# Performance work log

Measured on AMD Instinct MI355X. Metric: run time of the kernel, lower is better.

Reference implementation:

```python
import jax, jax.numpy as jnp
import numpy as np

NEG_SLOPE = 0.2
EPS = 1e-16


def gat_layer(x, src, dst, W, att_src, att_dst, bias, heads, out_ch, concat, n_nodes):
    # Linear projection -> [N, H, C]
    h = (x @ W).reshape(n_nodes, heads, out_ch)
    # Per-node attention logits [N, H]
    a_src = (h * att_src[None]).sum(-1)
    a_dst = (h * att_dst[None]).sum(-1)
    # Per-edge logits, LeakyReLU (message j -> i with src=j, dst=i)
    alpha = a_src[src] + a_dst[dst]                      # [E, H]
    alpha = jnp.where(alpha >= 0, alpha, NEG_SLOPE * alpha)
    # Segment softmax over incoming edges of each dst node
    amax = jax.ops.segment_max(alpha, dst, num_segments=n_nodes)  # [N, H]
    ealpha = jnp.exp(alpha - amax[dst])
    denom = jax.ops.segment_sum(ealpha, dst, num_segments=n_nodes)
    alpha = ealpha / (denom[dst] + EPS)
    # Weighted messages + scatter-add aggregation
    msg = h[src] * alpha[..., None]                      # [E, H, C]
    out = jax.ops.segment_sum(msg, dst, num_segments=n_nodes)  # [N, H, C]
    out = out.reshape(n_nodes, heads * out_ch) if concat else out.mean(axis=1)
    return out + bias


def setup_inputs() -> dict:
    key = jax.random.key(0)
    ks = jax.random.split(key, 11)
    N, E, F, H, C1 = 50000, 1600000, 128, 8, 8
    x = jax.random.normal(ks[0], (N, F), dtype=jnp.float32)
    edge_index = jax.random.randint(ks[1], (2, E), 0, N, dtype=jnp.int64)
    s = 1.0 / np.sqrt(F)
    W1 = jax.random.normal(ks[2], (F, H * C1), dtype=jnp.float32) * s
    att_src1 = jax.random.normal(ks[3], (H, C1), dtype=jnp.float32) * 0.1
    att_dst1 = jax.random.normal(ks[4], (H, C1), dtype=jnp.float32) * 0.1
    bias1 = jax.random.normal(ks[5], (H * C1,), dtype=jnp.float32) * 0.1
    W2 = jax.random.normal(ks[6], (H * C1, F), dtype=jnp.float32) * (1.0 / np.sqrt(H * C1))
    att_src2 = jax.random.normal(ks[7], (1, F), dtype=jnp.float32) * 0.1
    att_dst2 = jax.random.normal(ks[8], (1, F), dtype=jnp.float32) * 0.1
    bias2 = jax.random.normal(ks[9], (F,), dtype=jnp.float32) * 0.1
    return {"x": x, "edge_index": edge_index, "W1": W1, "att_src1": att_src1,
            "att_dst1": att_dst1, "bias1": bias1, "W2": W2, "att_src2": att_src2,
            "att_dst2": att_dst2, "bias2": bias2}


def reference(x, edge_index, W1, att_src1, att_dst1, bias1, W2, att_src2, att_dst2, bias2):
    N = x.shape[0]
    # PyG GATConv add_self_loops=True: append (i, i) for every node
    loops = jnp.arange(N, dtype=edge_index.dtype)
    src = jnp.concatenate([edge_index[0], loops])
    dst = jnp.concatenate([edge_index[1], loops])
    # eval mode: dropouts are identity
    h = gat_layer(x, src, dst, W1, att_src1, att_dst1, bias1, heads=8, out_ch=8,
                  concat=True, n_nodes=N)            # [N, 64]
    h = jax.nn.elu(h)
    out = gat_layer(h, src, dst, W2, att_src2, att_dst2, bias2, heads=1, out_ch=128,
                    concat=False, n_nodes=N)         # [N, 128]
    return out
```

## Files before the change

kernel.cpp:

```cpp
#include <hip/hip_runtime.h>
#include <stdint.h>

#define NEG_SLOPE 0.2f
#define EPSV 1e-16f
#define LOG2E 1.44269504088896340736f
#define NBLK 256
#define BCAP 12288
#define PKCAP 8192

typedef __attribute__((ext_vector_type(8))) _Float16 half8;
typedef __attribute__((ext_vector_type(4))) float f32x4;

__device__ inline void get_edge(const void* ei, int is64, int E, int e, int& s, int& d){
  if (e >= E){ s = d = e - E; return; }
  if (is64){
    const long long* p = (const long long*)ei;
    s = (int)p[e]; d = (int)p[(long long)E + e];
  } else {
    const int* p = (const int*)ei;
    s = p[e]; d = p[E + e];
  }
}

__global__ __launch_bounds__(256) void k1g(const void* ei,
                     const float* __restrict__ x,
                     const float* __restrict__ W1,
                     const float* __restrict__ att_s, const float* __restrict__ att_d,
                     _Float16* __restrict__ Cb,
                     float* __restrict__ asrc1, float* __restrict__ adst1, int M,
                     const float* __restrict__ W2, _Float16* __restrict__ W2p,
                     const float* __restrict__ as2, const float* __restrict__ ad2,
                     float* __restrict__ va_s, float* __restrict__ va_d,
                     int E, int E2, int GG,
                     int* __restrict__ gcnt,
                     unsigned* __restrict__ packed){
  __shared__ char smem[34*1024];
  int b = blockIdx.x, t = threadIdx.x;

  if (b < GG){
    _Float16* Bs = (_Float16*)smem;
#pragma unroll
    for (int r = 0; r < 32; ++r){
      int idx = r*256 + t;
      int j = idx & 7, n16 = (idx >> 3) & 15, q = (idx >> 7) & 3, tile = idx >> 9;
      int nt = tile & 3, kt = tile >> 2;
      int k = kt*32 + q*8 + j, n = nt*16 + n16;
      Bs[idx] = (_Float16)W1[k*64 + n];
    }
    __syncthreads();
    int wave = (b*256 + t) >> 6;
    int lane = t & 63;
    int row0 = wave << 4;
    if (row0 >= M) return;
    int m = lane & 15, q = lane >> 4;
    f32x4 acc[4];
#pragma unroll
    for (int i = 0; i < 4; ++i) acc[i] = (f32x4){0.f,0.f,0.f,0.f};
#pragma unroll
    for (int kt = 0; kt < 4; ++kt){
      const float* xr = x + (size_t)(row0 + m)*128 + kt*32 + q*8;
      f32x4 f0 = *(const f32x4*)xr;
      f32x4 f1 = *(const f32x4*)(xr + 4);
      half8 a;
#pragma unroll
      for (int j = 0; j < 4; ++j){ a[j] = (_Float16)f0[j]; a[4 + j] = (_Float16)f1[j]; }
#pragma unroll
      for (int nt = 0; nt < 4; ++nt){
        half8 bfr = *(const half8*)(Bs + (size_t)(((kt*4 + nt)*4 + q)*16 + m)*8);
        acc[nt] = __builtin_amdgcn_mfma_f32_16x16x32_f16(a, bfr, acc[nt], 0, 0, 0);
      }
    }
#pragma unroll
    for (int nt = 0; nt < 4; ++nt){
#pragma unroll
      for (int r = 0; r < 4; ++r){
        Cb[(size_t)(row0 + q*4 + r)*64 + nt*16 + m] = (_Float16)acc[nt][r];
      }
    }
    float atts[4], attd[4];
#pragma unroll
    for (int nt = 0; nt < 4; ++nt){
      atts[nt] = att_s[nt*16 + m] * LOG2E;
      attd[nt] = att_d[nt*16 + m] * LOG2E;
    }
    int isw = (m & 7) == 0;
#pragma unroll
    for (int r = 0; r < 4; ++r){
      int row = row0 + q*4 + r;
#pragma unroll
      for (int nt = 0; nt < 4; ++nt){
        float ps = acc[nt][r] * atts[nt];
        float pd = acc[nt][r] * attd[nt];
#pragma unroll
        for (int mm = 1; mm <= 4; mm <<= 1){
          ps += __shfl_xor(ps, mm, 64);
          pd += __shfl_xor(pd, mm, 64);
        }
        if (isw){
          int head = 2*nt + (m >> 3);
          asrc1[row*8 + head] = ps;
          adst1[row*8 + head] = pd;
        }
      }
    }
    return;
  }

  if (b == GG){
#pragma unroll
    for (int r = 0; r < 32; ++r){
      int idx = r*256 + t;
      int j = idx & 7, n16 = (idx >> 3) & 15, q = (idx >> 7) & 3, tile = idx >> 9;
      int nt = tile & 7, kt = tile >> 3;
      int k = kt*32 + q*8 + j, n = nt*16 + n16;
      W2p[idx] = (_Float16)W2[k*128 + n];
    }
    if (t < 64){
      float s = 0.f, d = 0.f;
      for (int c = 0; c < 128; ++c){
        float w = W2[t*128 + c];
        s = fmaf(w, as2[c], s);
        d = fmaf(w, ad2[c], d);
      }
      va_s[t] = s * LOG2E; va_d[t] = d * LOG2E;
    }
    return;
  }

  unsigned* pk = (unsigned*)smem;
  int* h   = (int*)(smem + 32*1024);
  int* cur = (int*)(smem + 33*1024);
  int blk = b - GG - 1;
  int chunk = (E2 + NBLK - 1)/NBLK;
  int beg = blk*chunk, end = min(beg + chunk, E2), cnt = end - beg;
  const int* e32 = (const int*)ei;
  int nz = 0;
  for (int i = 0; i < 64; ++i) nz |= e32[2*i + 1];
  int is64 = (nz == 0) ? 1 : 0;
  h[t] = 0; __syncthreads();
  for (int j = t; j < cnt; j += 256){
    int s, d; get_edge(ei, is64, E, beg + j, s, d);
    unsigned p = ((unsigned)s << 16) | (unsigned)d;
    pk[j] = p;
    atomicAdd(&h[(p >> 8) & 255u], 1);
  }
  __syncthreads();
  int mine = h[t];
  int base_t = 0;
  if (mine > 0) base_t = atomicAdd(&gcnt[t*16], mine);
  cur[t] = base_t;
  __syncthreads();
  for (int j = t; j < cnt; j += 256){
    unsigned p = pk[j];
    int bk = (p >> 8) & 255u;
    int pos = atomicAdd(&cur[bk], 1);
    packed[(size_t)bk*BCAP + pos] = p;
  }
}

__global__ __launch_bounds__(256) void gemm2(const _Float16* __restrict__ A, const _Float16* __restrict__ Bp,
                                             const float* __restrict__ bias,
                                             float* __restrict__ C, int M){
  constexpr int NKT = 2, NNT = 8;
  int wave = (blockIdx.x*256 + (int)threadIdx.x) >> 6;
  int lane = threadIdx.x & 63;
  int row0 = wave << 4;
  if (row0 >= M) return;
  int m = lane & 15, q = lane >> 4;
  f32x4 acc[NNT];
#pragma unroll
  for (int i = 0; i < NNT; ++i) acc[i] = (f32x4){0.f,0.f,0.f,0.f};
#pragma unroll
  for (int kt = 0; kt < NKT; ++kt){
    half8 a = *(const half8*)(A + (size_t)(row0 + m)*64 + kt*32 + q*8);
#pragma unroll
    for (int nt = 0; nt < NNT; ++nt){
      half8 b = *(const half8*)(Bp + (size_t)(((kt*NNT + nt)*4 + q)*16 + m)*8);
      acc[nt] = __builtin_amdgcn_mfma_f32_16x16x32_f16(a, b, acc[nt], 0, 0, 0);
    }
  }
#pragma unroll
  for (int nt = 0; nt < NNT; ++nt){
    float bv = bias[nt*16 + m];
#pragma unroll
    for (int r = 0; r < 4; ++r){
      C[(size_t)(row0 + q*4 + r)*128 + nt*16 + m] = acc[nt][r] + bv;
    }
  }
}

__global__ __launch_bounds__(256) void p4_sort(const unsigned* __restrict__ packed,
                                               const int* __restrict__ gcnt,
                                               int N, int E2,
                                               int* __restrict__ offs, int* __restrict__ srcs){
  __shared__ int hist[256];
  __shared__ int cur[256];
  __shared__ int tot[256];
  __shared__ int sbase, scnt;
  int b = blockIdx.x, t = threadIdx.x;
  int v0 = gcnt[t*16];
  tot[t] = v0; __syncthreads();
  for (int off = 1; off < 256; off <<= 1){
    int v = (t >= off) ? tot[t - off] : 0;
    __syncthreads(); tot[t] += v; __syncthreads();
  }
  if (t == b){ sbase = tot[t] - v0; scnt = v0; }
  __syncthreads();
  int base = sbase, cnt = scnt;
  hist[t] = 0; __syncthreads();
  const unsigned* bp = packed + (size_t)b*BCAP;
  for (int p = t; p < cnt; p += 256){
    atomicAdd(&hist[bp[p] & 255u], 1);
  }
  __syncthreads();
  int v = hist[t];
  cur[t] = v; __syncthreads();
  for (int off = 1; off < 256; off <<= 1){
    int u = (t >= off) ? cur[t - off] : 0;
    __syncthreads(); cur[t] += u; __syncthreads();
  }
  int ex = cur[t] - v;
  __syncthreads();
  cur[t] = ex;
  int node = b*256 + t;
  if (node < N) offs[node] = base + ex;
  __syncthreads();
  for (int p = t; p < cnt; p += 256){
    unsigned pk = bp[p];
    int pos = atomicAdd(&cur[pk & 255u], 1);
    srcs[base + pos] = (int)((pk >> 16) << 7);
  }
  if (b == 0 && t == 0) offs[N] = E2;
}

__global__ __launch_bounds__(256) void agg_l1(const char* __restrict__ h1b,
                       const float* __restrict__ asrc, const float* __restrict__ adst,
                       const int* __restrict__ offs, const int* __restrict__ srcs,
                       const float* __restrict__ bias,
                       const float* __restrict__ va_s, const float* __restrict__ va_d,
                       uint4* __restrict__ hout,
                       float* __restrict__ asrc2, float* __restrict__ adst2, int N){
  int tid = threadIdx.x;
  int i = blockIdx.x*4 + (tid >> 6);
  if (i >= N) return;
  int lane = tid & 63, g = lane >> 3, c = lane & 7;
  unsigned coff = (unsigned)(c << 4);
  float ad = adst[i*8 + c];
  int beg = offs[i], end = offs[i + 1], last = end - 1;
  float acc[8];
#pragma unroll
  for (int k = 0; k < 8; ++k) acc[k] = 0.f;
  float den = 0.f;
  float a[4]; half8 v[4];
  {
    unsigned so[4];
#pragma unroll
    for (int k = 0; k < 4; ++k) so[k] = (unsigned)srcs[min(beg + 8*k + g, last)];
#pragma unroll
    for (int k = 0; k < 4; ++k) a[k] = asrc[(so[k] >> 4) + (unsigned)c];
#pragma unroll
    for (int k = 0; k < 4; ++k) v[k] = *(const half8*)(h1b + (size_t)(so[k] + coff));
  }
  for (int p = beg; p < end; p += 32){
    int pn = p + 32;
    unsigned so_n[4]; float a_n[4]; half8 v_n[4];
#pragma unroll
    for (int k = 0; k < 4; ++k) so_n[k] = (unsigned)srcs[min(pn + 8*k + g, last)];
#pragma unroll
    for (int k = 0; k < 4; ++k) a_n[k] = asrc[(so_n[k] >> 4) + (unsigned)c];
#pragma unroll
    for (int k = 0; k < 4; ++k) v_n[k] = *(const half8*)(h1b + (size_t)(so_n[k] + coff));
    float w[4];
#pragma unroll
    for (int k = 0; k < 4; ++k){
      float z = a[k] + ad;
      z = fmaxf(z, NEG_SLOPE*z);
      w[k] = (p + 8*k + g < end) ? exp2f(z) : 0.f;
      den += w[k];
    }
#pragma unroll
    for (int k = 0; k < 4; ++k){
#pragma unroll
      for (int j = 0; j < 8; ++j){
        acc[j] = fmaf((float)v[k][j], w[k], acc[j]);
      }
    }
#pragma unroll
    for (int k = 0; k < 4; ++k){ a[k] = a_n[k]; v[k] = v_n[k]; }
  }
#pragma unroll
  for (int mm = 8; mm <= 32; mm <<= 1){
#pragma unroll
    for (int k = 0; k < 8; ++k) acc[k] += __shfl_xor(acc[k], mm, 64);
    den += __shfl_xor(den, mm, 64);
  }
  if (g == 0){
    float inv = 1.f/(den + EPSV);
    float o[8];
    union { _Float16 h[8]; uint4 u; } ov;
#pragma unroll
    for (int k = 0; k < 8; ++k){
      float t = acc[k]*inv + bias[c*8 + k];
      t = (t > 0.f) ? t : (__expf(t) - 1.f);
      o[k] = t;
      ov.h[k] = (_Float16)t;
    }
    hout[(size_t)i*8 + c] = ov.u;
    float ps = 0.f, pd = 0.f;
#pragma unroll
    for (int k = 0; k < 8; ++k){
      ps = fmaf(o[k], va_s[c*8 + k], ps);
      pd = fmaf(o[k], va_d[c*8 + k], pd);
    }
#pragma unroll
    for (int mm = 1; mm <= 4; mm <<= 1){
      ps += __shfl_xor(ps, mm, 8);
      pd += __shfl_xor(pd, mm, 8);
    }
    if (c == 0){ asrc2[i] = ps; adst2[i] = pd; }
  }
}

__global__ __launch_bounds__(256) void agg_l2(const char* __restrict__ hin2,
                       const float* __restrict__ asrc, const float* __restrict__ adst,
                       const int* __restrict__ offs, const int* __restrict__ srcs,
                       uint4* __restrict__ qout, int N){
  int tid = threadIdx.x;
  int i = blockIdx.x*4 + (tid >> 6);
  if (i >= N) return;
  int lane = tid & 63, g = lane >> 3, c = lane & 7;
  unsigned coff = (unsigned)(c << 4);
  float ad = adst[i];
  int beg = offs[i], end = offs[i + 1], last = end - 1;
  float acc[8];
#pragma unroll
  for (int k = 0; k < 8; ++k) acc[k] = 0.f;
  float den = 0.f;
  float a[4]; half8 v[4];
  {
    unsigned so[4];
#pragma unroll
    for (int k = 0; k < 4; ++k) so[k] = (unsigned)srcs[min(beg + 8*k + g, last)];
#pragma unroll
    for (int k = 0; k < 4; ++k) a[k] = asrc[so[k] >> 7];
#pragma unroll
    for (int k = 0; k < 4; ++k) v[k] = *(const half8*)(hin2 + (size_t)(so[k] + coff));
  }
  for (int p = beg; p < end; p += 32){
    int pn = p + 32;
    unsigned so_n[4]; float a_n[4]; half8 v_n[4];
#pragma unroll
    for (int k = 0; k < 4; ++k) so_n[k] = (unsigned)srcs[min(pn + 8*k + g, last)];
#pragma unroll
    for (int k = 0; k < 4; ++k) a_n[k] = asrc[so_n[k] >> 7];
#pragma unroll
    for (int k = 0; k < 4; ++k) v_n[k] = *(const half8*)(hin2 + (size_t)(so_n[k] + coff));
    float w[4];
#pragma unroll
    for (int k = 0; k < 4; ++k){
      float z = a[k] + ad;
      z = fmaxf(z, NEG_SLOPE*z);
      w[k] = (p + 8*k + g < end) ? exp2f(z) : 0.f;
      den += w[k];
    }
#pragma unroll
    for (int k = 0; k < 4; ++k){
#pragma unroll
      for (int j = 0; j < 8; ++j){
        acc[j] = fmaf((float)v[k][j], w[k], acc[j]);
      }
    }
#pragma unroll
    for (int k = 0; k < 4; ++k){ a[k] = a_n[k]; v[k] = v_n[k]; }
  }
#pragma unroll
  for (int mm = 8; mm <= 32; mm <<= 1){
#pragma unroll
    for (int k = 0; k < 8; ++k) acc[k] += __shfl_xor(acc[k], mm, 64);
    den += __shfl_xor(den, mm, 64);
  }
  if (g == 0){
    float inv = 1.f/(den + EPSV);
    union { _Float16 h[8]; uint4 u; } ov;
#pragma unroll
    for (int k = 0; k < 8; ++k) ov.h[k] = (_Float16)(acc[k]*inv);
    qout[(size_t)i*8 + c] = ov.u;
  }
}

extern "C" void kernel_launch(void* const* d_in, const int* in_sizes, int n_in,
                              void* d_out, int out_size, void* d_ws, size_t ws_size,
                              hipStream_t stream){
  const float* x   = (const float*)d_in[0];
  const void*  ei  = d_in[1];
  const float* W1  = (const float*)d_in[2];
  const float* as1 = (const float*)d_in[3];
  const float* ad1 = (const float*)d_in[4];
  const float* b1  = (const float*)d_in[5];
  const float* W2  = (const float*)d_in[6];
  const float* as2 = (const float*)d_in[7];
  const float* ad2 = (const float*)d_in[8];
  const float* b2  = (const float*)d_in[9];

  int N  = in_sizes[0] / 128;
  int E  = in_sizes[1] / 2;
  int E2 = E + N;
  int NB = (N + 255) >> 8;

  char* p = (char*)d_ws;
  auto alloc = [&](size_t bytes) -> void* {
    void* r = (void*)p;
    p += (bytes + 255) & ~(size_t)255;
    return r;
  };
  _Float16* W2p    = (_Float16*)alloc((size_t)64*128*2);
  _Float16* h1b    = (_Float16*)alloc((size_t)N*64*2);
  float*    asrc1  = (float*)alloc((size_t)N*8*4);
  float*    adst1  = (float*)alloc((size_t)N*8*4);
  _Float16* hin2   = (_Float16*)alloc((size_t)N*64*2);
  _Float16* hq     = (_Float16*)alloc((size_t)N*64*2);
  float*    asrc2  = (float*)alloc((size_t)N*4);
  float*    adst2  = (float*)alloc((size_t)N*4);
  float*    va_s2  = (float*)alloc(64*4);
  float*    va_d2  = (float*)alloc(64*4);
  int*      offs   = (int*)alloc((size_t)(N + 1)*4);
  int*      srcs   = (int*)alloc((size_t)E2*4);
  unsigned* packed = (unsigned*)alloc((size_t)256*BCAP*4);
  int*      gcnt   = (int*)alloc((size_t)256*16*4);

  dim3 B(256);
  hipMemsetAsync(gcnt, 0, (size_t)256*16*4, stream);

  int nwav = (N + 15)/16;
  int GG = (nwav + 3)/4;

  k1g<<<GG + 1 + NBLK, B, 0, stream>>>(ei, x, W1, as1, ad1, h1b, asrc1, adst1, N,
                                       W2, W2p, as2, ad2, va_s2, va_d2,
                                       E, E2, GG, gcnt, packed);

  p4_sort<<<NB, B, 0, stream>>>(packed, gcnt, N, E2, offs, srcs);

  agg_l1<<<(N + 3)/4, B, 0, stream>>>((const char*)h1b, asrc1, adst1, offs, srcs, b1,
                                      va_s2, va_d2, (uint4*)hin2, asrc2, adst2, N);

  agg_l2<<<(N + 3)/4, B, 0, stream>>>((const char*)hin2, asrc2, adst2, offs, srcs,
                                      (uint4*)hq, N);

  gemm2<<<(nwav + 3)/4, B, 0, stream>>>(hq, W2p, b2, (float*)d_out, N);
}
```

Baseline: 240.7 us.

## Fuse layer-2 aggregation with output projection and drop software prefetch

Merges the layer-2 aggregation kernel with the final 64x128 projection. Each block aggregates four nodes into shared memory, then computes the 128 outputs per node with scalar FMAs against a transposed fp16 W2, plus bias. This removes the intermediate fp16 buffer round trip and one kernel launch, but gives up the MFMA GEMM for scalar math. It also drops the register double-buffered prefetch of edge data in both aggregation loops, which lowers register pressure but may expose gather latency.

```diff
diff --git a/kernel.cpp b/kernel.cpp
--- a/kernel.cpp
+++ b/kernel.cpp
@@ -28,7 +28,7 @@
                      const float* __restrict__ att_s, const float* __restrict__ att_d,
                      _Float16* __restrict__ Cb,
                      float* __restrict__ asrc1, float* __restrict__ adst1, int M,
-                     const float* __restrict__ W2, _Float16* __restrict__ W2p,
+                     const float* __restrict__ W2, _Float16* __restrict__ W2t,
                      const float* __restrict__ as2, const float* __restrict__ ad2,
                      float* __restrict__ va_s, float* __restrict__ va_d,
                      int E, int E2, int GG,
@@ -110,10 +110,8 @@
 #pragma unroll
     for (int r = 0; r < 32; ++r){
       int idx = r*256 + t;
-      int j = idx & 7, n16 = (idx >> 3) & 15, q = (idx >> 7) & 3, tile = idx >> 9;
-      int nt = tile & 7, kt = tile >> 3;
-      int k = kt*32 + q*8 + j, n = nt*16 + n16;
-      W2p[idx] = (_Float16)W2[k*128 + n];
+      int j = idx >> 6, c = idx & 63;
+      W2t[idx] = (_Float16)W2[c*128 + j];
     }
     if (t < 64){
       float s = 0.f, d = 0.f;
@@ -158,37 +156,6 @@
   }
 }
 
-__global__ __launch_bounds__(256) void gemm2(const _Float16* __restrict__ A, const _Float16* __restrict__ Bp,
-                                             const float* __restrict__ bias,
-                                             float* __restrict__ C, int M){
-  constexpr int NKT = 2, NNT = 8;
-  int wave = (blockIdx.x*256 + (int)threadIdx.x) >> 6;
-  int lane = threadIdx.x & 63;
-  int row0 = wave << 4;
-  if (row0 >= M) return;
-  int m = lane & 15, q = lane >> 4;
-  f32x4 acc[NNT];
-#pragma unroll
-  for (int i = 0; i < NNT; ++i) acc[i] = (f32x4){0.f,0.f,0.f,0.f};
-#pragma unroll
-  for (int kt = 0; kt < NKT; ++kt){
-    half8 a = *(const half8*)(A + (size_t)(row0 + m)*64 + kt*32 + q*8);
-#pragma unroll
-    for (int nt = 0; nt < NNT; ++nt){
-      half8 b = *(const half8*)(Bp + (size_t)(((kt*NNT + nt)*4 + q)*16 + m)*8);
-      acc[nt] = __builtin_amdgcn_mfma_f32_16x16x32_f16(a, b, acc[nt], 0, 0, 0);
-    }
-  }
-#pragma unroll
-  for (int nt = 0; nt < NNT; ++nt){
-    float bv = bias[nt*16 + m];
-#pragma unroll
-    for (int r = 0; r < 4; ++r){
-      C[(size_t)(row0 + q*4 + r)*128 + nt*16 + m] = acc[nt][r] + bv;
-    }
-  }
-}
-
 __global__ __launch_bounds__(256) void p4_sort(const unsigned* __restrict__ packed,
                                                const int* __restrict__ gcnt,
                                                int N, int E2,
@@ -251,31 +218,24 @@
 #pragma unroll
   for (int k = 0; k < 8; ++k) acc[k] = 0.f;
   float den = 0.f;
-  float a[4]; half8 v[4];
-  {
-    unsigned so[4];
-#pragma unroll
-    for (int k = 0; k < 4; ++k) so[k] = (unsigned)srcs[min(beg + 8*k + g, last)];
+  for (int p = beg; p < end; p += 32){
+    int m[4]; unsigned so[4];
+#pragma unroll
+    for (int k = 0; k < 4; ++k) m[k] = p + 8*k + g;
+#pragma unroll
+    for (int k = 0; k < 4; ++k) so[k] = (unsigned)srcs[min(m[k], last)];
+    float a[4];
 #pragma unroll
     for (int k = 0; k < 4; ++k) a[k] = asrc[(so[k] >> 4) + (unsigned)c];
+    half8 v[4];
 #pragma unroll
     for (int k = 0; k < 4; ++k) v[k] = *(const half8*)(h1b + (size_t)(so[k] + coff));
-  }
-  for (int p = beg; p < end; p += 32){
-    int pn = p + 32;
-    unsigned so_n[4]; float a_n[4]; half8 v_n[4];
-#pragma unroll
-    for (int k = 0; k < 4; ++k) so_n[k] = (unsigned)srcs[min(pn + 8*k + g, last)];
-#pragma unroll
-    for (int k = 0; k < 4; ++k) a_n[k] = asrc[(so_n[k] >> 4) + (unsigned)c];
-#pragma unroll
-    for (int k = 0; k < 4; ++k) v_n[k] = *(const half8*)(h1b + (size_t)(so_n[k] + coff));
     float w[4];
 #pragma unroll
     for (int k = 0; k < 4; ++k){
       float z = a[k] + ad;
       z = fmaxf(z, NEG_SLOPE*z);
-      w[k] = (p + 8*k + g < end) ? exp2f(z) : 0.f;
+      w[k] = (m[k] < end) ? exp2f(z) : 0.f;
       den += w[k];
     }
 #pragma unroll
@@ -285,8 +245,6 @@
         acc[j] = fmaf((float)v[k][j], w[k], acc[j]);
       }
     }
-#pragma unroll
-    for (int k = 0; k < 4; ++k){ a[k] = a_n[k]; v[k] = v_n[k]; }
   }
 #pragma unroll
   for (int mm = 8; mm <= 32; mm <<= 1){
@@ -321,71 +279,82 @@
   }
 }
 
-__global__ __launch_bounds__(256) void agg_l2(const char* __restrict__ hin2,
+__global__ __launch_bounds__(256) void agg2g(const char* __restrict__ hin2,
                        const float* __restrict__ asrc, const float* __restrict__ adst,
                        const int* __restrict__ offs, const int* __restrict__ srcs,
-                       uint4* __restrict__ qout, int N){
+                       const _Float16* __restrict__ W2t, const float* __restrict__ bias,
+                       float* __restrict__ C, int N){
+  __shared__ float qs[4][64];
   int tid = threadIdx.x;
-  int i = blockIdx.x*4 + (tid >> 6);
-  if (i >= N) return;
+  int node = tid >> 6;
+  int i = blockIdx.x*4 + node;
   int lane = tid & 63, g = lane >> 3, c = lane & 7;
-  unsigned coff = (unsigned)(c << 4);
-  float ad = adst[i];
-  int beg = offs[i], end = offs[i + 1], last = end - 1;
-  float acc[8];
-#pragma unroll
-  for (int k = 0; k < 8; ++k) acc[k] = 0.f;
-  float den = 0.f;
-  float a[4]; half8 v[4];
-  {
-    unsigned so[4];
-#pragma unroll
-    for (int k = 0; k < 4; ++k) so[k] = (unsigned)srcs[min(beg + 8*k + g, last)];
-#pragma unroll
-    for (int k = 0; k < 4; ++k) a[k] = asrc[so[k] >> 7];
-#pragma unroll
-    for (int k = 0; k < 4; ++k) v[k] = *(const half8*)(hin2 + (size_t)(so[k] + coff));
-  }
-  for (int p = beg; p < end; p += 32){
-    int pn = p + 32;
-    unsigned so_n[4]; float a_n[4]; half8 v_n[4];
-#pragma unroll
-    for (int k = 0; k < 4; ++k) so_n[k] = (unsigned)srcs[min(pn + 8*k + g, last)];
-#pragma unroll
-    for (int k = 0; k < 4; ++k) a_n[k] = asrc[so_n[k] >> 7];
-#pragma unroll
-    for (int k = 0; k < 4; ++k) v_n[k] = *(const half8*)(hin2 + (size_t)(so_n[k] + coff));
-    float w[4];
-#pragma unroll
-    for (int k = 0; k < 4; ++k){
-      float z = a[k] + ad;
-      z = fmaxf(z, NEG_SLOPE*z);
-      w[k] = (p + 8*k + g < end) ? exp2f(z) : 0.f;
-      den += w[k];
-    }
-#pragma unroll
-    for (int k = 0; k < 4; ++k){
-#pragma unroll
-      for (int j = 0; j < 8; ++j){
-        acc[j] = fmaf((float)v[k][j], w[k], acc[j]);
-      }
-    }
-#pragma unroll
-    for (int k = 0; k < 4; ++k){ a[k] = a_n[k]; v[k] = v_n[k]; }
-  }
-#pragma unroll
-  for (int mm = 8; mm <= 32; mm <<= 1){
-#pragma unroll
-    for (int k = 0; k < 8; ++k) acc[k] += __shfl_xor(acc[k], mm, 64);
-    den += __shfl_xor(den, mm, 64);
-  }
-  if (g == 0){
-    float inv = 1.f/(den + EPSV);
-    union { _Float16 h[8]; uint4 u; } ov;
-#pragma unroll
-    for (int k = 0; k < 8; ++k) ov.h[k] = (_Float16)(acc[k]*inv);
-    qout[(size_t)i*8 + c] = ov.u;
-  }
+  if (i < N){
+    unsigned coff = (unsigned)(c << 4);
+    float ad = adst[i];
+    int beg = offs[i], end = offs[i + 1], last = end - 1;
+    float acc[8];
+#pragma unroll
+    for (int k = 0; k < 8; ++k) acc[k] = 0.f;
+    float den = 0.f;
+    for (int p = beg; p < end; p += 32){
+      int m[4]; unsigned so[4];
+#pragma unroll
+      for (int k = 0; k < 4; ++k) m[k] = p + 8*k + g;
+#pragma unroll
+      for (int k = 0; k < 4; ++k) so[k] = (unsigned)srcs[min(m[k], last)];
+      float a[4];
+#pragma unroll
+      for (int k = 0; k < 4; ++k) a[k] = asrc[so[k] >> 7];
+      half8 v[4];
+#pragma unroll
+      for (int k = 0; k < 4; ++k) v[k] = *(const half8*)(hin2 + (size_t)(so[k] + coff));
+      float w[4];
+#pragma unroll
+      for (int k = 0; k < 4; ++k){
+        float z = a[k] + ad;
+        z = fmaxf(z, NEG_SLOPE*z);
+        w[k] = (m[k] < end) ? exp2f(z) : 0.f;
+        den += w[k];
+      }
+#pragma unroll
+      for (int k = 0; k < 4; ++k){
+#pragma unroll
+        for (int j = 0; j < 8; ++j){
+          acc[j] = fmaf((float)v[k][j], w[k], acc[j]);
+        }
+      }
+    }
+#pragma unroll
+    for (int mm = 8; mm <= 32; mm <<= 1){
+#pragma unroll
+      for (int k = 0; k < 8; ++k) acc[k] += __shfl_xor(acc[k], mm, 64);
+      den += __shfl_xor(den, mm, 64);
+    }
+    if (g == 0){
+      float inv = 1.f/(den + EPSV);
+#pragma unroll
+      for (int k = 0; k < 8; ++k) qs[node][c*8 + k] = acc[k]*inv;
+    }
+  }
+  __syncthreads();
+  int j = tid & 127, hb = tid >> 7;
+  int n0 = hb*2;
+  float d0 = 0.f, d1 = 0.f;
+#pragma unroll
+  for (int q8 = 0; q8 < 8; ++q8){
+    half8 wv = *(const half8*)(W2t + (size_t)j*64 + q8*8);
+#pragma unroll
+    for (int k = 0; k < 8; ++k){
+      float wf = (float)wv[k];
+      d0 = fmaf(qs[n0][q8*8 + k],     wf, d0);
+      d1 = fmaf(qs[n0 + 1][q8*8 + k], wf, d1);
+    }
+  }
+  float bv = bias[j];
+  int i0 = blockIdx.x*4 + n0;
+  if (i0 < N)     C[(size_t)i0*128 + j]       = d0 + bv;
+  if (i0 + 1 < N) C[(size_t)(i0 + 1)*128 + j] = d1 + bv;
 }
 
 extern "C" void kernel_launch(void* const* d_in, const int* in_sizes, int n_in,
@@ -413,12 +382,11 @@
     p += (bytes + 255) & ~(size_t)255;
     return r;
   };
-  _Float16* W2p    = (_Float16*)alloc((size_t)64*128*2);
+  _Float16* W2t    = (_Float16*)alloc((size_t)128*64*2);
   _Float16* h1b    = (_Float16*)alloc((size_t)N*64*2);
   float*    asrc1  = (float*)alloc((size_t)N*8*4);
   float*    adst1  = (float*)alloc((size_t)N*8*4);
   _Float16* hin2   = (_Float16*)alloc((size_t)N*64*2);
-  _Float16* hq     = (_Float16*)alloc((size_t)N*64*2);
   float*    asrc2  = (float*)alloc((size_t)N*4);
   float*    adst2  = (float*)alloc((size_t)N*4);
   float*    va_s2  = (float*)alloc(64*4);
@@ -435,7 +403,7 @@
   int GG = (nwav + 3)/4;
 
   k1g<<<GG + 1 + NBLK, B, 0, stream>>>(ei, x, W1, as1, ad1, h1b, asrc1, adst1, N,
-                                       W2, W2p, as2, ad2, va_s2, va_d2,
+                                       W2, W2t, as2, ad2, va_s2, va_d2,
                                        E, E2, GG, gcnt, packed);
 
   p4_sort<<<NB, B, 0, stream>>>(packed, gcnt, N, E2, offs, srcs);
@@ -443,8 +411,6 @@
   agg_l1<<<(N + 3)/4, B, 0, stream>>>((const char*)h1b, asrc1, adst1, offs, srcs, b1,
                                       va_s2, va_d2, (uint4*)hin2, asrc2, adst2, N);
 
-  agg_l2<<<(N + 3)/4, B, 0, stream>>>((const char*)hin2, asrc2, adst2, offs, srcs,
-                                      (uint4*)hq, N);
-
-  gemm2<<<(nwav + 3)/4, B, 0, stream>>>(hq, W2p, b2, (float*)d_out, N);
-}
+  agg2g<<<(N + 3)/4, B, 0, stream>>>((const char*)hin2, asrc2, adst2, offs, srcs,
+                                     W2t, b2, (float*)d_out, N);
+}
```

After: 301.1 us. 25.1% more time.
